# Kernel tuning notes

Hardware: AMD Instinct MI355X
Metric: run time of the kernel (lower is better)

Reference implementation:

```python
import jax, jax.numpy as jnp
import numpy as np

K_POW = 3.0
EPS = 1e-6

def _weight1(d, r):
    # (1 - (d/r)^2)^k for d < r else 0; guard base before float power
    base = jnp.where(d < r, 1.0 - (d / r) ** 2, 0.0)
    return base ** K_POW

def _weight2(d, r):
    # 1 for d < r/2; (1 - ((2d-r)/r)^2)^k for r/2 <= d < r; else 0
    band = (d >= r / 2) & (d < r)
    base = jnp.where(band, 1.0 - ((2.0 * d - r) / r) ** 2, 0.0)
    return jnp.where(d < r / 2, 1.0, base ** K_POW)

def setup_inputs() -> dict:
    key = jax.random.key(0)
    ks = jax.random.split(key, 10)
    n, p, L = 4096, 128, 32
    x = jax.random.uniform(ks[0], (n, p), dtype=jnp.float32)
    s = 0.05
    return {
        "x": x,
        "r0": jnp.float32(4.0),
        "r1": jnp.float32(2.0),
        "r2": jnp.float32(4.0),
        "We1": jax.random.normal(ks[1], (L, p), jnp.float32) * s,
        "be1": jnp.zeros((L,), jnp.float32),
        "We2": jax.random.normal(ks[2], (L, L), jnp.float32) * s,
        "be2": jnp.zeros((L,), jnp.float32),
        "Wd1": jax.random.normal(ks[3], (L, L), jnp.float32) * s,
        "bd1": jnp.zeros((L,), jnp.float32),
        "Wd2": jax.random.normal(ks[4], (p, L), jnp.float32) * s,
        "bd2": jnp.zeros((p,), jnp.float32),
    }

def _mr_layer(x, r0, r1, r2):
    y = x  # y = x.clone()
    x2 = jnp.sum(x * x, axis=-1)
    d2 = x2[:, None] + x2[None, :] - 2.0 * (x @ x.T)  # (n, n)
    dist = jnp.sqrt(jnp.maximum(d2, 1e-12))
    md = dist.max()
    # torch reassigns r to max_dist when r > max_dist -> min(r, max_dist)
    r0e = jnp.minimum(r0, md)
    r1e = jnp.minimum(r1, md)
    r2e = jnp.minimum(r2, md)
    # inds = any(dist <= r0) is all-true (diag is ~0), so no row selection needed
    alpha = _weight1(dist, r0e)
    alpha = alpha / jnp.sum(alpha, axis=0, keepdims=True)
    mu = alpha.T @ x  # (n, p)
    mu = jnp.where(jnp.isnan(mu), y, mu)
    U = y - mu  # (n, p); contraction direction per point
    # projection scalar ps[i,j] = <x_i - y_j, U_j>, avoiding (n,n,p) diff tensor
    ps = x @ U.T - jnp.sum(y * U, axis=-1)[None, :]  # (n, n)
    u_norm2 = jnp.sum(U * U, axis=-1)[None, :]  # (1, n)
    dist_u2 = jnp.maximum(ps ** 2 * u_norm2, EPS)
    dist_v = jnp.sqrt(jnp.maximum(dist ** 2 - dist_u2, EPS))
    dist_u = jnp.sqrt(dist_u2)
    beta = _weight2(dist_v, r1e) * _weight2(dist_u, r2e)
    beta = beta / jnp.sum(beta, axis=0, keepdims=True)
    e_Z = beta.T @ x
    e_Z = jnp.where(jnp.isnan(e_Z), y, e_Z)
    return e_Z

def reference(x, r0, r1, r2, We1, be1, We2, be2, Wd1, bd1, Wd2, bd2):
    y = _mr_layer(x, r0, r1, r2)
    # encoder: Linear -> GELU(exact) -> Linear
    h = jax.nn.gelu(y @ We1.T + be1, approximate=False)
    z = h @ We2.T + be2
    # decoder: Linear -> GELU(exact) -> Linear -> Sigmoid
    h2 = jax.nn.gelu(z @ Wd1.T + bd1, approximate=False)
    x_hat = jax.nn.sigmoid(h2 @ Wd2.T + bd2)
    # loss = lam_recon * MSE(x, x_hat); lam_topo = lam_geom = 0
    return jnp.mean((x - x_hat) ** 2)
```

## Files before the change

kernel.cpp:

```cpp
#include <hip/hip_runtime.h>
#include <math.h>

#define N 4096
#define P 128
#define LDIM 32
#define CHUNKS 8
#define ITILES 4

typedef unsigned int u32;
typedef unsigned short u16;
typedef short s16x8 __attribute__((ext_vector_type(8)));
typedef float f32x4 __attribute__((ext_vector_type(4)));

__device__ __forceinline__ u16 f2b(float f) {
  u32 u = __float_as_uint(f);
  u += 0x7fffu + ((u >> 16) & 1u);
  return (u16)(u >> 16);
}
__device__ __forceinline__ float b2f(u16 h) { return __uint_as_float(((u32)h) << 16); }

__device__ __forceinline__ float geluf(float a) {
  return 0.5f * a * (1.0f + erff(a * 0.70710678118654752f));
}

#define MFMA(a, b, c) __builtin_amdgcn_mfma_f32_16x16x32_bf16((a), (b), (c), 0, 0, 0)

__global__ void k_init(u32* __restrict__ mdb, float* __restrict__ out) {
  if (threadIdx.x == 0) { *mdb = 0u; out[0] = 0.0f; }
}

__global__ __launch_bounds__(256) void k_prep(const float* __restrict__ x, u16* __restrict__ xb,
                                              u16* __restrict__ xbT, float* __restrict__ x2) {
  __shared__ u16 tlT[128][40];
  const int bi = blockIdx.x * 32;
  const int tid = threadIdx.x;
  const int r = tid >> 3, cg = (tid & 7) * 16;
  const float* src = &x[(size_t)(bi + r) * P + cg];
  float4 v0 = *(const float4*)(src + 0);
  float4 v1 = *(const float4*)(src + 4);
  float4 v2 = *(const float4*)(src + 8);
  float4 v3 = *(const float4*)(src + 12);
  u16 h[16];
  h[0] = f2b(v0.x); h[1] = f2b(v0.y); h[2] = f2b(v0.z); h[3] = f2b(v0.w);
  h[4] = f2b(v1.x); h[5] = f2b(v1.y); h[6] = f2b(v1.z); h[7] = f2b(v1.w);
  h[8] = f2b(v2.x); h[9] = f2b(v2.y); h[10] = f2b(v2.z); h[11] = f2b(v2.w);
  h[12] = f2b(v3.x); h[13] = f2b(v3.y); h[14] = f2b(v3.z); h[15] = f2b(v3.w);
  float s = 0.0f;
#pragma unroll
  for (int e = 0; e < 16; e++) { float f = b2f(h[e]); s = fmaf(f, f, s); }
  s += __shfl_down(s, 4); s += __shfl_down(s, 2); s += __shfl_down(s, 1);
  if ((tid & 7) == 0) x2[bi + r] = s;
  uint4 p0, p1;
  p0.x = (u32)h[0] | ((u32)h[1] << 16);  p0.y = (u32)h[2] | ((u32)h[3] << 16);
  p0.z = (u32)h[4] | ((u32)h[5] << 16);  p0.w = (u32)h[6] | ((u32)h[7] << 16);
  p1.x = (u32)h[8] | ((u32)h[9] << 16);  p1.y = (u32)h[10] | ((u32)h[11] << 16);
  p1.z = (u32)h[12] | ((u32)h[13] << 16); p1.w = (u32)h[14] | ((u32)h[15] << 16);
  *(uint4*)&xb[(size_t)(bi + r) * P + cg] = p0;
  *(uint4*)&xb[(size_t)(bi + r) * P + cg + 8] = p1;
#pragma unroll
  for (int e = 0; e < 16; e++) tlT[cg + e][r] = h[e];
  __syncthreads();
  const int c = tid >> 1, hh = tid & 1;
  uint4 q0 = *(const uint4*)&tlT[c][hh * 16];
  uint4 q1 = *(const uint4*)&tlT[c][hh * 16 + 8];
  *(uint4*)&xbT[(size_t)c * N + bi + hh * 16] = q0;
  *(uint4*)&xbT[(size_t)c * N + bi + hh * 16 + 8] = q1;
}

__global__ __launch_bounds__(128) void k_anchor(const u16* __restrict__ xb, const float* __restrict__ x2,
                                                u32* __restrict__ mdb) {
  const int i = blockIdx.x * 128 + threadIdx.x;
  const uint4* ra = (const uint4*)(xb + (size_t)i * P);
  const uint4* r0 = (const uint4*)xb;
  float dot = 0.0f;
#pragma unroll
  for (int q = 0; q < 16; ++q) {
    uint4 a = ra[q], b = r0[q];
    u32 aa[4] = {a.x, a.y, a.z, a.w}, bb[4] = {b.x, b.y, b.z, b.w};
#pragma unroll
    for (int e = 0; e < 4; e++) {
      dot = fmaf(b2f((u16)(aa[e] & 0xffffu)), b2f((u16)(bb[e] & 0xffffu)), dot);
      dot = fmaf(b2f((u16)(aa[e] >> 16)), b2f((u16)(bb[e] >> 16)), dot);
    }
  }
  float d2 = fmaxf(x2[i] + x2[0] - 2.0f * dot, 0.0f);
#pragma unroll
  for (int o = 32; o > 0; o >>= 1) d2 = fmaxf(d2, __shfl_down(d2, o));
  if ((threadIdx.x & 63) == 0) atomicMax(mdb, __float_as_uint(d2));
}

__global__ __launch_bounds__(512, 4) void k_grammax(const u16* __restrict__ xb, const float* __restrict__ x2,
                                                    u32* __restrict__ mdb,
                                                    const float* __restrict__ r0p, const float* __restrict__ r1p,
                                                    const float* __restrict__ r2p) {
  const float rmax = fmaxf(r0p[0], fmaxf(r1p[0], r2p[0])) * 1.02f;
  if (__uint_as_float(*mdb) >= rmax * rmax) return;
  __shared__ uint4 LA[1024];
  const int j0 = blockIdx.x * 64;
  const int cid = blockIdx.y;
  if (cid * 512 + 512 <= j0) return;
  const int tid = threadIdx.x;
  const int lane = tid & 63, w = tid >> 6;
  const int lm = lane & 15, quad = lane >> 4;
  {
    const uint4* g = (const uint4*)(xb + (size_t)j0 * P);
#pragma unroll
    for (int it = 0; it < 2; ++it) {
      int c = it * 512 + tid;
      int row = c >> 4, ch = c & 15;
      LA[row * 16 + (ch ^ (row & 7))] = g[c];
    }
  }
  float x2j[4][4];
#pragma unroll
  for (int u = 0; u < 4; u++)
#pragma unroll
    for (int reg = 0; reg < 4; reg++) x2j[u][reg] = x2[j0 + u * 16 + quad * 4 + reg];
  __syncthreads();
  float lmax = 0.0f;
  for (int t = 0; t < ITILES; ++t) {
    const int i0 = cid * 512 + t * 128;
    if (i0 + 128 <= j0) continue;
    f32x4 accG[4];
#pragma unroll
    for (int u = 0; u < 4; u++) accG[u] = {0.f, 0.f, 0.f, 0.f};
    const u16* gb = xb + (size_t)(i0 + w * 16 + lm) * P;
#pragma unroll
    for (int ks = 0; ks < 4; ++ks) {
      s16x8 bf = *(const s16x8*)(gb + ks * 32 + quad * 8);
      s16x8 af[4];
#pragma unroll
      for (int u = 0; u < 4; u++) { int m = u * 16 + lm; af[u] = *(const s16x8*)&LA[m * 16 + ((ks * 4 + quad) ^ (m & 7))]; }
#pragma unroll
      for (int u = 0; u < 4; u++) accG[u] = MFMA(af[u], bf, accG[u]);
    }
    float x2i = x2[i0 + w * 16 + lm];
#pragma unroll
    for (int u = 0; u < 4; u++)
#pragma unroll
      for (int reg = 0; reg < 4; reg++) lmax = fmaxf(lmax, x2j[u][reg] + x2i - 2.0f * accG[u][reg]);
  }
#pragma unroll
  for (int o = 32; o > 0; o >>= 1) lmax = fmaxf(lmax, __shfl_down(lmax, o));
  if (lane == 0) atomicMax(mdb, __float_as_uint(lmax));
}

__global__ __launch_bounds__(512, 4) void k_alpha(const u16* __restrict__ xb, const u16* __restrict__ xbT,
                                                  const float* __restrict__ x2,
                                                  float* __restrict__ muP, float* __restrict__ S1P,
                                                  const float* __restrict__ r0p, const u32* __restrict__ mdb) {
  __shared__ uint4 LA[1024];
  __shared__ u16 W16[64 * 136];
  __shared__ float S1L[64];
  const int j0 = blockIdx.x * 64, cid = blockIdx.y;
  const int tid = threadIdx.x;
  const int lane = tid & 63, w = tid >> 6;
  const int lm = lane & 15, quad = lane >> 4;
  {
    const uint4* g = (const uint4*)(xb + (size_t)j0 * P);
#pragma unroll
    for (int it = 0; it < 2; ++it) {
      int c = it * 512 + tid;
      int row = c >> 4, ch = c & 15;
      LA[row * 16 + (ch ^ (row & 7))] = g[c];
    }
  }
  if (tid < 64) S1L[tid] = 0.0f;
  const float mdf = sqrtf(fmaxf(__uint_as_float(*mdb), 1e-12f));
  const float re = fminf(r0p[0], mdf);
  const float re2 = re * re, inv_re2 = 1.0f / re2;
  float x2j[4];
#pragma unroll
  for (int v = 0; v < 4; v++) x2j[v] = x2[j0 + v * 16 + lm];
  f32x4 accPV[4];
#pragma unroll
  for (int u = 0; u < 4; u++) accPV[u] = {0.f, 0.f, 0.f, 0.f};
  float sjv[4] = {0.f, 0.f, 0.f, 0.f};
  __syncthreads();
  for (int t = 0; t < ITILES; ++t) {
    const int i0 = (cid * ITILES + t) * 128;
    f32x4 accG[4];
#pragma unroll
    for (int v = 0; v < 4; v++) accG[v] = {0.f, 0.f, 0.f, 0.f};
    const u16* ga = xb + (size_t)(i0 + w * 16 + lm) * P;
#pragma unroll
    for (int ks = 0; ks < 4; ++ks) {
      s16x8 af = *(const s16x8*)(ga + ks * 32 + quad * 8);
      s16x8 bf[4];
#pragma unroll
      for (int v = 0; v < 4; v++) { int m = v * 16 + lm; bf[v] = *(const s16x8*)&LA[m * 16 + ((ks * 4 + quad) ^ (m & 7))]; }
#pragma unroll
      for (int v = 0; v < 4; v++) accG[v] = MFMA(af, bf[v], accG[v]);
    }
    float4 x2iv = *(const float4*)&x2[i0 + w * 16 + quad * 4];
    const float xi[4] = {x2iv.x, x2iv.y, x2iv.z, x2iv.w};
    u16 wv4[4][4];
#pragma unroll
    for (int v = 0; v < 4; v++)
#pragma unroll
      for (int reg = 0; reg < 4; reg++) {
        float d2 = fmaxf(xi[reg] + x2j[v] - 2.0f * accG[v][reg], 1e-12f);
        float wt = 0.0f;
        if (d2 < re2) { float b = 1.0f - d2 * inv_re2; wt = b * b * b; }
        sjv[v] += wt;
        wv4[v][reg] = f2b(wt);
      }
    __syncthreads();
#pragma unroll
    for (int v = 0; v < 4; v++) {
      ushort4 pk; pk.x = wv4[v][0]; pk.y = wv4[v][1]; pk.z = wv4[v][2]; pk.w = wv4[v][3];
      *(ushort4*)&W16[(v * 16 + lm) * 136 + w * 16 + quad * 4] = pk;
    }
    __syncthreads();
    const u16* gx = xbT + (size_t)(w * 16 + lm) * N + i0;
#pragma unroll
    for (int ks = 0; ks < 4; ++ks) {
      s16x8 bx = *(const s16x8*)(gx + ks * 32 + quad * 8);
      s16x8 aw[4];
#pragma unroll
      for (int u = 0; u < 4; u++) { int m = u * 16 + lm; aw[u] = *(const s16x8*)&W16[m * 136 + ks * 32 + quad * 8]; }
#pragma unroll
      for (int u = 0; u < 4; u++) accPV[u] = MFMA(aw[u], bx, accPV[u]);
    }
  }
  float* mu = muP + (size_t)cid * N * P;
#pragma unroll
  for (int u = 0; u < 4; u++)
#pragma unroll
    for (int reg = 0; reg < 4; reg++)
      __builtin_nontemporal_store(accPV[u][reg],
        &mu[(size_t)(j0 + u * 16 + quad * 4 + reg) * P + w * 16 + lm]);
#pragma unroll
  for (int v = 0; v < 4; v++) atomicAdd(&S1L[v * 16 + lm], sjv[v]);
  __syncthreads();
  if (tid < 64) S1P[cid * N + j0 + tid] = S1L[tid];
}

__global__ __launch_bounds__(128) void k_finU(const float* __restrict__ x, const u16* __restrict__ xb,
                                              const float* __restrict__ muP, const float* __restrict__ S1P,
                                              u16* __restrict__ Ub, float* __restrict__ u2, float* __restrict__ cj) {
  const int j = blockIdx.x, t = threadIdx.x;
  float ssum = 0.0f, msum = 0.0f;
#pragma unroll
  for (int c = 0; c < CHUNKS; ++c) {
    ssum += S1P[c * N + j];
    msum += __builtin_nontemporal_load(&muP[((size_t)c * N + j) * P + t]);
  }
  float xv = x[(size_t)j * P + t];
  float uval = 0.0f;
  if (ssum > 0.0f) uval = xv - msum / ssum;
  u16 ub = f2b(uval);
  Ub[(size_t)j * P + t] = ub;
  float uf = b2f(ub);
  float xbf = b2f(xb[(size_t)j * P + t]);
  float a = uf * uf, b = xbf * uf;
#pragma unroll
  for (int o = 32; o > 0; o >>= 1) { a += __shfl_down(a, o); b += __shfl_down(b, o); }
  __shared__ float ra[2], rb[2];
  if ((t & 63) == 0) { ra[t >> 6] = a; rb[t >> 6] = b; }
  __syncthreads();
  if (t == 0) { u2[j] = ra[0] + ra[1]; cj[j] = rb[0] + rb[1]; }
}

__global__ __launch_bounds__(512, 4) void k_betaez(const u16* __restrict__ xb, const u16* __restrict__ Ub,
                                                   const u16* __restrict__ xbT,
                                                   const float* __restrict__ x2, const float* __restrict__ u2,
                                                   const float* __restrict__ cj,
                                                   float* __restrict__ ezP, float* __restrict__ S2P,
                                                   const float* __restrict__ r1p, const float* __restrict__ r2p,
                                                   const u32* __restrict__ mdb) {
  __shared__ uint4 LA[1024];
  __shared__ uint4 LU[1024];
  __shared__ u16 W16[64 * 136];
  __shared__ float S2L[64];
  const int j0 = blockIdx.x * 64, cid = blockIdx.y;
  const int tid = threadIdx.x;
  const int lane = tid & 63, w = tid >> 6;
  const int lm = lane & 15, quad = lane >> 4;
  {
    const uint4* ga = (const uint4*)(xb + (size_t)j0 * P);
    const uint4* gu = (const uint4*)(Ub + (size_t)j0 * P);
#pragma unroll
    for (int it = 0; it < 2; ++it) {
      int c = it * 512 + tid;
      int row = c >> 4, ch = c & 15;
      int sw = row * 16 + (ch ^ (row & 7));
      LA[sw] = ga[c];
      LU[sw] = gu[c];
    }
  }
  if (tid < 64) S2L[tid] = 0.0f;
  const float mdf = sqrtf(fmaxf(__uint_as_float(*mdb), 1e-12f));
  const float r1e = fminf(r1p[0], mdf), r2e = fminf(r2p[0], mdf);
  const float r1q = r1e * r1e, r1h = 0.25f * r1q;
  const float r2q = r2e * r2e, r2h = 0.25f * r2q;
  const float inv_r1 = 1.0f / r1e, inv_r2 = 1.0f / r2e;
  float x2j[4], u2j[4], ncj[4];
#pragma unroll
  for (int v = 0; v < 4; v++) {
    int jj = j0 + v * 16 + lm;
    x2j[v] = x2[jj]; u2j[v] = u2[jj]; ncj[v] = -cj[jj];
  }
  f32x4 accPV[4];
#pragma unroll
  for (int u = 0; u < 4; u++) accPV[u] = {0.f, 0.f, 0.f, 0.f};
  float sjv[4] = {0.f, 0.f, 0.f, 0.f};
  __syncthreads();
  for (int t = 0; t < ITILES; ++t) {
    const int i0 = (cid * ITILES + t) * 128;
    f32x4 accG[4], accP[4];
#pragma unroll
    for (int v = 0; v < 4; v++) {
      accG[v] = {0.f, 0.f, 0.f, 0.f};
      accP[v] = {ncj[v], ncj[v], ncj[v], ncj[v]};
    }
    const u16* ga = xb + (size_t)(i0 + w * 16 + lm) * P;
#pragma unroll
    for (int ks = 0; ks < 4; ++ks) {
      s16x8 af = *(const s16x8*)(ga + ks * 32 + quad * 8);
      s16x8 bf[4], bu[4];
#pragma unroll
      for (int v = 0; v < 4; v++) {
        int m = v * 16 + lm;
        int off = m * 16 + ((ks * 4 + quad) ^ (m & 7));
        bf[v] = *(const s16x8*)&LA[off];
        bu[v] = *(const s16x8*)&LU[off];
      }
#pragma unroll
      for (int v = 0; v < 4; v++) {
        accG[v] = MFMA(af, bf[v], accG[v]);
        accP[v] = MFMA(af, bu[v], accP[v]);
      }
    }
    float4 x2iv = *(const float4*)&x2[i0 + w * 16 + quad * 4];
    const float xi[4] = {x2iv.x, x2iv.y, x2iv.z, x2iv.w};
    u16 wv4[4][4];
#pragma unroll
    for (int v = 0; v < 4; v++)
#pragma unroll
      for (int reg = 0; reg < 4; reg++) {
        float d2 = fmaxf(xi[reg] + x2j[v] - 2.0f * accG[v][reg], 1e-12f);
        float ps = accP[v][reg];
        float du2 = fmaxf(ps * ps * u2j[v], 1e-6f);
        float dv2 = fmaxf(d2 - du2, 1e-6f);
        float wt;
        if (dv2 >= r1q || du2 >= r2q) {
          wt = 0.0f;
        } else if (dv2 < r1h && du2 < r2h) {
          wt = 1.0f;
        } else {
          float wa = 1.0f;
          if (dv2 >= r1h) { float dv = sqrtf(dv2); float tt = 2.0f * dv * inv_r1 - 1.0f; float b = 1.0f - tt * tt; wa = b * b * b; }
          float wb = 1.0f;
          if (du2 >= r2h) { float du = sqrtf(du2); float tt = 2.0f * du * inv_r2 - 1.0f; float b = 1.0f - tt * tt; wb = b * b * b; }
          wt = wa * wb;
        }
        sjv[v] += wt;
        wv4[v][reg] = f2b(wt);
      }
    __syncthreads();
#pragma unroll
    for (int v = 0; v < 4; v++) {
      ushort4 pk; pk.x = wv4[v][0]; pk.y = wv4[v][1]; pk.z = wv4[v][2]; pk.w = wv4[v][3];
      *(ushort4*)&W16[(v * 16 + lm) * 136 + w * 16 + quad * 4] = pk;
    }
    __syncthreads();
    const u16* gx = xbT + (size_t)(w * 16 + lm) * N + i0;
#pragma unroll
    for (int ks = 0; ks < 4; ++ks) {
      s16x8 bx = *(const s16x8*)(gx + ks * 32 + quad * 8);
      s16x8 aw[4];
#pragma unroll
      for (int u = 0; u < 4; u++) { int m = u * 16 + lm; aw[u] = *(const s16x8*)&W16[m * 136 + ks * 32 + quad * 8]; }
#pragma unroll
      for (int u = 0; u < 4; u++) accPV[u] = MFMA(aw[u], bx, accPV[u]);
    }
  }
  float* ez = ezP + (size_t)cid * N * P;
#pragma unroll
  for (int u = 0; u < 4; u++)
#pragma unroll
    for (int reg = 0; reg < 4; reg++)
      __builtin_nontemporal_store(accPV[u][reg],
        &ez[(size_t)(j0 + u * 16 + quad * 4 + reg) * P + w * 16 + lm]);
#pragma unroll
  for (int v = 0; v < 4; v++) atomicAdd(&S2L[v * 16 + lm], sjv[v]);
  __syncthreads();
  if (tid < 64) S2P[cid * N + j0 + tid] = S2L[tid];
}

#define AE_ROWS 16
__global__ __launch_bounds__(256) void k_ae(const float* __restrict__ x, const float* __restrict__ ezP,
                                            const float* __restrict__ S2P,
                                            const float* __restrict__ We1, const float* __restrict__ be1,
                                            const float* __restrict__ We2, const float* __restrict__ be2,
                                            const float* __restrict__ Wd1, const float* __restrict__ bd1,
                                            const float* __restrict__ Wd2, const float* __restrict__ bd2,
                                            float* __restrict__ out) {
  __shared__ float We1T[P][33];
  __shared__ float We2T[LDIM][33];
  __shared__ float Wd1T[LDIM][33];
  __shared__ float Wd2T[LDIM][129];
  __shared__ float ezs[AE_ROWS][P];
  __shared__ float h1s[AE_ROWS][LDIM], zbs[AE_ROWS][LDIM], h2s[AE_ROWS][LDIM];
  __shared__ float be1s[LDIM], be2s[LDIM], bd1s[LDIM], bd2s[P];
  __shared__ float s2s[AE_ROWS];
  const int tid = threadIdx.x;
  const int r0 = blockIdx.x * AE_ROWS;
  for (int idx = tid; idx < P * LDIM; idx += 256) {
    int o = idx >> 7, k = idx & 127;
    We1T[k][o] = We1[idx];
    int o2 = idx >> 5, k2 = idx & 31;
    Wd2T[k2][o2] = Wd2[idx];
  }
  for (int idx = tid; idx < LDIM * LDIM; idx += 256) {
    int o = idx >> 5, k = idx & 31;
    We2T[k][o] = We2[idx];
    Wd1T[k][o] = Wd1[idx];
  }
  if (tid < LDIM) { be1s[tid] = be1[tid]; be2s[tid] = be2[tid]; bd1s[tid] = bd1[tid]; }
  if (tid < P) bd2s[tid] = bd2[tid];
  if (tid < AE_ROWS) {
    float s = 0.0f;
#pragma unroll
    for (int c = 0; c < CHUNKS; ++c) s += S2P[c * N + r0 + tid];
    s2s[tid] = s;
  }
  __syncthreads();
  for (int idx = tid; idx < AE_ROWS * P; idx += 256) {
    int r = idx >> 7, col = idx & 127;
    int row = r0 + r;
    float es = 0.0f;
#pragma unroll
    for (int c = 0; c < CHUNKS; ++c) es += __builtin_nontemporal_load(&ezP[((size_t)c * N + row) * P + col]);
    float xv = x[(size_t)row * P + col];
    ezs[r][col] = (s2s[r] > 0.0f) ? (es / s2s[r]) : xv;
  }
  __syncthreads();
  {
    const int o = tid & 31, rh = tid >> 5;
#pragma unroll
    for (int rr = 0; rr < 2; rr++) {
      int r = rh + rr * 8;
      float a = be1s[o];
#pragma unroll 8
      for (int k = 0; k < P; k++) a = fmaf(We1T[k][o], ezs[r][k], a);
      h1s[r][o] = geluf(a);
    }
  }
  __syncthreads();
  {
    const int o = tid & 31, rh = tid >> 5;
#pragma unroll
    for (int rr = 0; rr < 2; rr++) {
      int r = rh + rr * 8;
      float a = be2s[o];
#pragma unroll
      for (int k = 0; k < LDIM; k++) a = fmaf(We2T[k][o], h1s[r][k], a);
      zbs[r][o] = a;
    }
  }
  __syncthreads();
  {
    const int o = tid & 31, rh = tid >> 5;
#pragma unroll
    for (int rr = 0; rr < 2; rr++) {
      int r = rh + rr * 8;
      float a = bd1s[o];
#pragma unroll
      for (int k = 0; k < LDIM; k++) a = fmaf(Wd1T[k][o], zbs[r][k], a);
      h2s[r][o] = geluf(a);
    }
  }
  __syncthreads();
  {
    const int o = tid & 127, rh = tid >> 7;
    float part = 0.0f;
#pragma unroll
    for (int rr = 0; rr < 8; rr++) {
      int r = rh + rr * 2;
      int row = r0 + r;
      float a = bd2s[o];
#pragma unroll
      for (int k = 0; k < LDIM; k++) a = fmaf(Wd2T[k][o], h2s[r][k], a);
      float xh = 1.0f / (1.0f + expf(-a));
      float diff = x[(size_t)row * P + o] - xh;
      part = fmaf(diff, diff, part);
    }
#pragma unroll
    for (int off = 32; off > 0; off >>= 1) part += __shfl_down(part, off);
    if ((tid & 63) == 0) atomicAdd(out, part * (1.0f / ((float)N * (float)P)));
  }
}

extern "C" void kernel_launch(void* const* d_in, const int* in_sizes, int n_in,
                              void* d_out, int out_size, void* d_ws, size_t ws_size,
                              hipStream_t stream) {
  const float* x   = (const float*)d_in[0];
  const float* r0  = (const float*)d_in[1];
  const float* r1  = (const float*)d_in[2];
  const float* r2  = (const float*)d_in[3];
  const float* We1 = (const float*)d_in[4];
  const float* be1 = (const float*)d_in[5];
  const float* We2 = (const float*)d_in[6];
  const float* be2 = (const float*)d_in[7];
  const float* Wd1 = (const float*)d_in[8];
  const float* bd1 = (const float*)d_in[9];
  const float* Wd2 = (const float*)d_in[10];
  const float* bd2 = (const float*)d_in[11];
  float* out = (float*)d_out;

  char* base = (char*)d_ws;
  size_t off = 0;
  u16* xb  = (u16*)(base + off); off += (size_t)N * P * 2;
  u16* xbT = (u16*)(base + off); off += (size_t)N * P * 2;
  u16* Ub  = (u16*)(base + off); off += (size_t)N * P * 2;
  float* muP = (float*)(base + off); off += (size_t)CHUNKS * N * P * 4;
  float* ezP = (float*)(base + off); off += (size_t)CHUNKS * N * P * 4;
  float* S1P = (float*)(base + off); off += (size_t)CHUNKS * N * 4;
  float* S2P = (float*)(base + off); off += (size_t)CHUNKS * N * 4;
  float* x2  = (float*)(base + off); off += (size_t)N * 4;
  u32* mdb   = (u32*)(base + off); off += 4;
  float* u2  = (float*)(base + off); off += (size_t)N * 4;
  float* cjv = (float*)(base + off); off += (size_t)N * 4;

  hipLaunchKernelGGL(k_init, dim3(1), dim3(64), 0, stream, mdb, out);
  hipLaunchKernelGGL(k_prep, dim3(N / 32), dim3(256), 0, stream, x, xb, xbT, x2);
  hipLaunchKernelGGL(k_anchor, dim3(N / 128), dim3(128), 0, stream, xb, x2, mdb);
  hipLaunchKernelGGL(k_grammax, dim3(N / 64, CHUNKS), dim3(512), 0, stream, xb, x2, mdb, r0, r1, r2);
  hipLaunchKernelGGL(k_alpha, dim3(N / 64, CHUNKS), dim3(512), 0, stream, xb, xbT, x2, muP, S1P, r0, mdb);
  hipLaunchKernelGGL(k_finU, dim3(N), dim3(128), 0, stream, x, xb, muP, S1P, Ub, u2, cjv);
  hipLaunchKernelGGL(k_betaez, dim3(N / 64, CHUNKS), dim3(512), 0, stream, xb, Ub, xbT, x2, u2, cjv, ezP, S2P, r1, r2, mdb);
  hipLaunchKernelGGL(k_ae, dim3(N / AE_ROWS), dim3(256), 0, stream, x, ezP, S2P, We1, be1, We2, be2, Wd1, bd1, Wd2, bd2, out);
}
```

Baseline: 175.0 us.

## Split alpha/beta i-ranges finer and skip all-zero beta tiles in weighted sums

Raises the i-dimension split count for the alpha pass and the beta/e_Z pass, with uneven tile counts per chunk in beta, and relaxes launch bounds to allow more occupancy. In the beta pass, each tile checks whether every bf16 weight is zero and, if so, skips the LDS write, barrier and MFMA accumulation. Chunks with no nonzero weight skip their partial-sum store, and per-chunk flags let the autoencoder kernel skip reading those partials. This adds a barrier, a ballot and flag traffic per tile, plus more partial buffers to reduce in finU and ae.

```diff
diff --git a/kernel.cpp b/kernel.cpp
--- a/kernel.cpp
+++ b/kernel.cpp
@@ -4,8 +4,8 @@
 #define N 4096
 #define P 128
 #define LDIM 32
-#define CHUNKS 8
-#define ITILES 4
+#define CHA 16
+#define CHB 12
 
 typedef unsigned int u32;
 typedef unsigned short u16;
@@ -25,7 +25,9 @@
 
 #define MFMA(a, b, c) __builtin_amdgcn_mfma_f32_16x16x32_bf16((a), (b), (c), 0, 0, 0)
 
-__global__ void k_init(u32* __restrict__ mdb, float* __restrict__ out) {
+__global__ __launch_bounds__(256) void k_init(u32* __restrict__ mdb, u32* __restrict__ ezflag,
+                                              float* __restrict__ out) {
+  for (int i = threadIdx.x; i < CHB * 64; i += 256) ezflag[i] = 0u;
   if (threadIdx.x == 0) { *mdb = 0u; out[0] = 0.0f; }
 }
 
@@ -118,7 +120,7 @@
     for (int reg = 0; reg < 4; reg++) x2j[u][reg] = x2[j0 + u * 16 + quad * 4 + reg];
   __syncthreads();
   float lmax = 0.0f;
-  for (int t = 0; t < ITILES; ++t) {
+  for (int t = 0; t < 4; ++t) {
     const int i0 = cid * 512 + t * 128;
     if (i0 + 128 <= j0) continue;
     f32x4 accG[4];
@@ -145,7 +147,7 @@
   if (lane == 0) atomicMax(mdb, __float_as_uint(lmax));
 }
 
-__global__ __launch_bounds__(512, 4) void k_alpha(const u16* __restrict__ xb, const u16* __restrict__ xbT,
+__global__ __launch_bounds__(512, 8) void k_alpha(const u16* __restrict__ xb, const u16* __restrict__ xbT,
                                                   const float* __restrict__ x2,
                                                   float* __restrict__ muP, float* __restrict__ S1P,
                                                   const float* __restrict__ r0p, const u32* __restrict__ mdb) {
@@ -177,8 +179,9 @@
   for (int u = 0; u < 4; u++) accPV[u] = {0.f, 0.f, 0.f, 0.f};
   float sjv[4] = {0.f, 0.f, 0.f, 0.f};
   __syncthreads();
-  for (int t = 0; t < ITILES; ++t) {
-    const int i0 = (cid * ITILES + t) * 128;
+#pragma unroll
+  for (int t = 0; t < 2; ++t) {
+    const int i0 = (cid * 2 + t) * 128;
     f32x4 accG[4];
 #pragma unroll
     for (int v = 0; v < 4; v++) accG[v] = {0.f, 0.f, 0.f, 0.f};
@@ -242,7 +245,7 @@
   const int j = blockIdx.x, t = threadIdx.x;
   float ssum = 0.0f, msum = 0.0f;
 #pragma unroll
-  for (int c = 0; c < CHUNKS; ++c) {
+  for (int c = 0; c < CHA; ++c) {
     ssum += S1P[c * N + j];
     msum += __builtin_nontemporal_load(&muP[((size_t)c * N + j) * P + t]);
   }
@@ -262,17 +265,19 @@
   if (t == 0) { u2[j] = ra[0] + ra[1]; cj[j] = rb[0] + rb[1]; }
 }
 
-__global__ __launch_bounds__(512, 4) void k_betaez(const u16* __restrict__ xb, const u16* __restrict__ Ub,
+__global__ __launch_bounds__(512, 6) void k_betaez(const u16* __restrict__ xb, const u16* __restrict__ Ub,
                                                    const u16* __restrict__ xbT,
                                                    const float* __restrict__ x2, const float* __restrict__ u2,
                                                    const float* __restrict__ cj,
                                                    float* __restrict__ ezP, float* __restrict__ S2P,
+                                                   u32* __restrict__ ezflag,
                                                    const float* __restrict__ r1p, const float* __restrict__ r2p,
                                                    const u32* __restrict__ mdb) {
   __shared__ uint4 LA[1024];
   __shared__ uint4 LU[1024];
   __shared__ u16 W16[64 * 136];
   __shared__ float S2L[64];
+  __shared__ u32 Wfl[8];
   const int j0 = blockIdx.x * 64, cid = blockIdx.y;
   const int tid = threadIdx.x;
   const int lane = tid & 63, w = tid >> 6;
@@ -305,9 +310,12 @@
 #pragma unroll
   for (int u = 0; u < 4; u++) accPV[u] = {0.f, 0.f, 0.f, 0.f};
   float sjv[4] = {0.f, 0.f, 0.f, 0.f};
-  __syncthreads();
-  for (int t = 0; t < ITILES; ++t) {
-    const int i0 = (cid * ITILES + t) * 128;
+  bool blockAny = false;
+  const int tstart = (cid < 8) ? cid * 3 : 24 + (cid - 8) * 2;
+  const int tcnt = (cid < 8) ? 3 : 2;
+  __syncthreads();
+  for (int t = 0; t < tcnt; ++t) {
+    const int i0 = (tstart + t) * 128;
     f32x4 accG[4], accP[4];
 #pragma unroll
     for (int v = 0; v < 4; v++) {
@@ -335,6 +343,7 @@
     float4 x2iv = *(const float4*)&x2[i0 + w * 16 + quad * 4];
     const float xi[4] = {x2iv.x, x2iv.y, x2iv.z, x2iv.w};
     u16 wv4[4][4];
+    u32 nz = 0u;
 #pragma unroll
     for (int v = 0; v < 4; v++)
 #pragma unroll
@@ -356,33 +365,45 @@
           wt = wa * wb;
         }
         sjv[v] += wt;
-        wv4[v][reg] = f2b(wt);
+        u16 hv = f2b(wt);
+        wv4[v][reg] = hv;
+        nz |= hv;
       }
+    if (lane == 0) Wfl[w] = 0u;
+    bool wany = __any(nz != 0u);
+    if (lane == 0 && wany) Wfl[w] = 1u;
     __syncthreads();
-#pragma unroll
-    for (int v = 0; v < 4; v++) {
-      ushort4 pk; pk.x = wv4[v][0]; pk.y = wv4[v][1]; pk.z = wv4[v][2]; pk.w = wv4[v][3];
-      *(ushort4*)&W16[(v * 16 + lm) * 136 + w * 16 + quad * 4] = pk;
-    }
-    __syncthreads();
-    const u16* gx = xbT + (size_t)(w * 16 + lm) * N + i0;
-#pragma unroll
-    for (int ks = 0; ks < 4; ++ks) {
-      s16x8 bx = *(const s16x8*)(gx + ks * 32 + quad * 8);
-      s16x8 aw[4];
-#pragma unroll
-      for (int u = 0; u < 4; u++) { int m = u * 16 + lm; aw[u] = *(const s16x8*)&W16[m * 136 + ks * 32 + quad * 8]; }
-#pragma unroll
-      for (int u = 0; u < 4; u++) accPV[u] = MFMA(aw[u], bx, accPV[u]);
-    }
-  }
-  float* ez = ezP + (size_t)cid * N * P;
-#pragma unroll
-  for (int u = 0; u < 4; u++)
-#pragma unroll
-    for (int reg = 0; reg < 4; reg++)
-      __builtin_nontemporal_store(accPV[u][reg],
-        &ez[(size_t)(j0 + u * 16 + quad * 4 + reg) * P + w * 16 + lm]);
+    u32 tileAny = Wfl[0] | Wfl[1] | Wfl[2] | Wfl[3] | Wfl[4] | Wfl[5] | Wfl[6] | Wfl[7];
+    if (tileAny) {
+      blockAny = true;
+#pragma unroll
+      for (int v = 0; v < 4; v++) {
+        ushort4 pk; pk.x = wv4[v][0]; pk.y = wv4[v][1]; pk.z = wv4[v][2]; pk.w = wv4[v][3];
+        *(ushort4*)&W16[(v * 16 + lm) * 136 + w * 16 + quad * 4] = pk;
+      }
+      __syncthreads();
+      const u16* gx = xbT + (size_t)(w * 16 + lm) * N + i0;
+#pragma unroll
+      for (int ks = 0; ks < 4; ++ks) {
+        s16x8 bx = *(const s16x8*)(gx + ks * 32 + quad * 8);
+        s16x8 aw[4];
+#pragma unroll
+        for (int u = 0; u < 4; u++) { int m = u * 16 + lm; aw[u] = *(const s16x8*)&W16[m * 136 + ks * 32 + quad * 8]; }
+#pragma unroll
+        for (int u = 0; u < 4; u++) accPV[u] = MFMA(aw[u], bx, accPV[u]);
+      }
+    }
+  }
+  if (blockAny) {
+    float* ez = ezP + (size_t)cid * N * P;
+#pragma unroll
+    for (int u = 0; u < 4; u++)
+#pragma unroll
+      for (int reg = 0; reg < 4; reg++)
+        __builtin_nontemporal_store(accPV[u][reg],
+          &ez[(size_t)(j0 + u * 16 + quad * 4 + reg) * P + w * 16 + lm]);
+    if (tid == 0) ezflag[cid * 64 + blockIdx.x] = 1u;
+  }
 #pragma unroll
   for (int v = 0; v < 4; v++) atomicAdd(&S2L[v * 16 + lm], sjv[v]);
   __syncthreads();
@@ -391,7 +412,7 @@
 
 #define AE_ROWS 16
 __global__ __launch_bounds__(256) void k_ae(const float* __restrict__ x, const float* __restrict__ ezP,
-                                            const float* __restrict__ S2P,
+                                            const float* __restrict__ S2P, const u32* __restrict__ ezflag,
                                             const float* __restrict__ We1, const float* __restrict__ be1,
                                             const float* __restrict__ We2, const float* __restrict__ be2,
                                             const float* __restrict__ Wd1, const float* __restrict__ bd1,
@@ -405,8 +426,10 @@
   __shared__ float h1s[AE_ROWS][LDIM], zbs[AE_ROWS][LDIM], h2s[AE_ROWS][LDIM];
   __shared__ float be1s[LDIM], be2s[LDIM], bd1s[LDIM], bd2s[P];
   __shared__ float s2s[AE_ROWS];
+  __shared__ u32 efl[CHB];
   const int tid = threadIdx.x;
   const int r0 = blockIdx.x * AE_ROWS;
+  const int jt = r0 >> 6;
   for (int idx = tid; idx < P * LDIM; idx += 256) {
     int o = idx >> 7, k = idx & 127;
     We1T[k][o] = We1[idx];
@@ -420,11 +443,13 @@
   }
   if (tid < LDIM) { be1s[tid] = be1[tid]; be2s[tid] = be2[tid]; bd1s[tid] = bd1[tid]; }
   if (tid < P) bd2s[tid] = bd2[tid];
-  if (tid < AE_ROWS) {
+  if (tid < CHB) efl[tid] = ezflag[tid * 64 + jt];
+  if (tid >= 128 && tid < 128 + AE_ROWS) {
+    int r = tid - 128;
     float s = 0.0f;
 #pragma unroll
-    for (int c = 0; c < CHUNKS; ++c) s += S2P[c * N + r0 + tid];
-    s2s[tid] = s;
+    for (int c = 0; c < CHB; ++c) s += S2P[c * N + r0 + r];
+    s2s[r] = s;
   }
   __syncthreads();
   for (int idx = tid; idx < AE_ROWS * P; idx += 256) {
@@ -432,7 +457,8 @@
     int row = r0 + r;
     float es = 0.0f;
 #pragma unroll
-    for (int c = 0; c < CHUNKS; ++c) es += __builtin_nontemporal_load(&ezP[((size_t)c * N + row) * P + col]);
+    for (int c = 0; c < CHB; ++c)
+      if (efl[c]) es += __builtin_nontemporal_load(&ezP[((size_t)c * N + row) * P + col]);
     float xv = x[(size_t)row * P + col];
     ezs[r][col] = (s2s[r] > 0.0f) ? (es / s2s[r]) : xv;
   }
@@ -515,21 +541,22 @@
   u16* xb  = (u16*)(base + off); off += (size_t)N * P * 2;
   u16* xbT = (u16*)(base + off); off += (size_t)N * P * 2;
   u16* Ub  = (u16*)(base + off); off += (size_t)N * P * 2;
-  float* muP = (float*)(base + off); off += (size_t)CHUNKS * N * P * 4;
-  float* ezP = (float*)(base + off); off += (size_t)CHUNKS * N * P * 4;
-  float* S1P = (float*)(base + off); off += (size_t)CHUNKS * N * 4;
-  float* S2P = (float*)(base + off); off += (size_t)CHUNKS * N * 4;
+  float* muP = (float*)(base + off); off += (size_t)CHA * N * P * 4;
+  float* ezP = (float*)(base + off); off += (size_t)CHB * N * P * 4;
+  float* S1P = (float*)(base + off); off += (size_t)CHA * N * 4;
+  float* S2P = (float*)(base + off); off += (size_t)CHB * N * 4;
   float* x2  = (float*)(base + off); off += (size_t)N * 4;
   u32* mdb   = (u32*)(base + off); off += 4;
+  u32* ezflag = (u32*)(base + off); off += (size_t)CHB * 64 * 4;
   float* u2  = (float*)(base + off); off += (size_t)N * 4;
   float* cjv = (float*)(base + off); off += (size_t)N * 4;
 
-  hipLaunchKernelGGL(k_init, dim3(1), dim3(64), 0, stream, mdb, out);
+  hipLaunchKernelGGL(k_init, dim3(1), dim3(256), 0, stream, mdb, ezflag, out);
   hipLaunchKernelGGL(k_prep, dim3(N / 32), dim3(256), 0, stream, x, xb, xbT, x2);
   hipLaunchKernelGGL(k_anchor, dim3(N / 128), dim3(128), 0, stream, xb, x2, mdb);
-  hipLaunchKernelGGL(k_grammax, dim3(N / 64, CHUNKS), dim3(512), 0, stream, xb, x2, mdb, r0, r1, r2);
-  hipLaunchKernelGGL(k_alpha, dim3(N / 64, CHUNKS), dim3(512), 0, stream, xb, xbT, x2, muP, S1P, r0, mdb);
+  hipLaunchKernelGGL(k_grammax, dim3(N / 64, 8), dim3(512), 0, stream, xb, x2, mdb, r0, r1, r2);
+  hipLaunchKernelGGL(k_alpha, dim3(N / 64, CHA), dim3(512), 0, stream, xb, xbT, x2, muP, S1P, r0, mdb);
   hipLaunchKernelGGL(k_finU, dim3(N), dim3(128), 0, stream, x, xb, muP, S1P, Ub, u2, cjv);
-  hipLaunchKernelGGL(k_betaez, dim3(N / 64, CHUNKS), dim3(512), 0, stream, xb, Ub, xbT, x2, u2, cjv, ezP, S2P, r1, r2, mdb);
-  hipLaunchKernelGGL(k_ae, dim3(N / AE_ROWS), dim3(256), 0, stream, x, ezP, S2P, We1, be1, We2, be2, Wd1, bd1, Wd2, bd2, out);
-}
+  hipLaunchKernelGGL(k_betaez, dim3(N / 64, CHB), dim3(512), 0, stream, xb, Ub, xbT, x2, u2, cjv, ezP, S2P, ezflag, r1, r2, mdb);
+  hipLaunchKernelGGL(k_ae, dim3(N / AE_ROWS), dim3(256), 0, stream, x, ezP, S2P, ezflag, We1, be1, We2, be2, Wd1, bd1, Wd2, bd2, out);
+}
```

After: 214.6 us. 1.23x slower.
